# Optimization experiments

Measured on AMD Instinct MI355X. Metric: run time of the kernel, lower is better.

The kernel has to match this reference:

```python
import jax, jax.numpy as jnp
import numpy as np

DIM = 1024
STATE = 256
B, S = 4, 4096

def setup_inputs() -> dict:
    key = jax.random.key(0)
    ks = jax.random.split(key, 8)
    sc_b = 1.0 / np.sqrt(DIM)
    sc_c = 1.0 / np.sqrt(STATE)
    return {
        "x": jax.random.normal(ks[0], (B, S, DIM), dtype=jnp.float32),
        "A": jax.random.normal(ks[1], (STATE,), dtype=jnp.float32) * 0.02,
        "B_w": jax.random.uniform(ks[2], (STATE, DIM), minval=-sc_b, maxval=sc_b),
        "B_b": jax.random.uniform(ks[3], (STATE,), minval=-sc_b, maxval=sc_b),
        "C_w": jax.random.uniform(ks[4], (DIM, STATE), minval=-sc_c, maxval=sc_c),
        "C_b": jax.random.uniform(ks[5], (DIM,), minval=-sc_c, maxval=sc_c),
        "D_w": jax.random.uniform(ks[6], (DIM, DIM), minval=-sc_b, maxval=sc_b),
        "D_b": jax.random.uniform(ks[7], (DIM,), minval=-sc_b, maxval=sc_b),
    }

def reference(x, A, B_w, B_b, C_w, C_b, D_w, D_b):
    # Precompute input projections in batch (the per-step loop only needs state*A + Bu)
    Bu = jnp.einsum('bsd,nd->bsn', x, B_w) + B_b          # [B,S,STATE]
    Du = jnp.einsum('bsd,ed->bse', x, D_w) + D_b          # [B,S,DIM]
    Aexp = jnp.exp(A)[None, :]                             # [1,STATE]
    state0 = jnp.zeros((x.shape[0], A.shape[0]), dtype=x.dtype)

    def step(state, bu_t):
        state = jnp.tanh(state * Aexp + bu_t)
        return state, state

    _, states = jax.lax.scan(step, state0, jnp.swapaxes(Bu, 0, 1))  # [S,B,STATE]
    states = jnp.swapaxes(states, 0, 1)                              # [B,S,STATE]
    y = jnp.einsum('bsn,en->bse', states, C_w) + C_b + Du
    return y
```

## Files before the change

kernel.cpp:

```cpp
#include <hip/hip_runtime.h>
#include <hip/hip_bf16.h>

#define DIM 1024
#define STATE 256
#define BATCH 4
#define SEQ 4096
#define M_TOT (BATCH * SEQ)

typedef short short8 __attribute__((ext_vector_type(8)));
typedef float f32x4 __attribute__((ext_vector_type(4)));

__device__ __forceinline__ unsigned short f2bf(float f) {
  unsigned int u = __float_as_uint(f);
  u += 0x7fff + ((u >> 16) & 1);
  return (unsigned short)(u >> 16);
}

__device__ __forceinline__ void gl_lds16(const void* g, void* l) {
  __builtin_amdgcn_global_load_lds(
      (const __attribute__((address_space(1))) void*)g,
      (__attribute__((address_space(3))) void*)l, 16, 0, 0);
}

#define C2F 2.8853900817779268f
#define LOG2EF 1.4426950408889634f
#define VMC(N) asm volatile("s_waitcnt vmcnt(" #N ")" ::: "memory")

__global__ __launch_bounds__(256) void convert_w(
    const float* __restrict__ A, const float* __restrict__ Bw,
    const float* __restrict__ Bb, const float* __restrict__ Cw,
    const float* __restrict__ Cb, const float* __restrict__ Dw,
    const float* __restrict__ Db, unsigned short* __restrict__ bwb,
    unsigned short* __restrict__ wob, float* __restrict__ bb2,
    float* __restrict__ mP2, float* __restrict__ cbdb) {
  const int bx = blockIdx.x;
  const int t = threadIdx.x;
  if (bx < 256) {
    int c = t * 4;
    const float4 v = *(const float4*)(Bw + (size_t)bx * DIM + c);
    *(ushort4*)(bwb + (size_t)bx * DIM + c) =
        make_ushort4(f2bf(v.x), f2bf(v.y), f2bf(v.z), f2bf(v.w));
  } else if (bx < 256 + 1024) {
    int e = bx - 256;
    if (t < 64) {
      const float4 v = *(const float4*)(Cw + (size_t)e * STATE + t * 4);
      *(ushort4*)(wob + (size_t)e * 1280 + t * 4) =
          make_ushort4(f2bf(v.x), f2bf(v.y), f2bf(v.z), f2bf(v.w));
    }
    const float4 v = *(const float4*)(Dw + (size_t)e * DIM + t * 4);
    *(ushort4*)(wob + (size_t)e * 1280 + 256 + t * 4) =
        make_ushort4(f2bf(v.x), f2bf(v.y), f2bf(v.z), f2bf(v.w));
  } else {
    const float P = C2F * __builtin_amdgcn_exp2f(A[t] * LOG2EF);
    bb2[t] = fmaf(Bb[t], C2F, P);
    mP2[t] = -2.0f * P;
#pragma unroll
    for (int k = 0; k < 4; ++k) {
      const int i = t * 4 + k;
      cbdb[i] = Cb[i] + Db[i];
    }
  }
}

__global__ __launch_bounds__(256, 3) void gemm_GX(
    const float* __restrict__ x,
    const unsigned short* __restrict__ bwb,
    float* __restrict__ G,
    const float* __restrict__ bb2,
    unsigned short* __restrict__ xb)
{
  __shared__ char AsB[32768];
  __shared__ char BsB[16384];

  const int tid = threadIdx.x;
  const int wave = tid >> 6;
  const int lane = tid & 63;
  const int lr = lane & 15;
  const int lk = lane >> 4;
  const int wr = wave >> 1;
  const int wc = wave & 1;

  const int bs = (blockIdx.x & 7) * 32 + (blockIdx.x >> 3);
  const int mtile = bs >> 1;
  const int ntile = bs & 1;
  const int m0 = mtile * 128;
  const int n0 = ntile * 128;

  f32x4 acc[4][4];
#pragma unroll
  for (int i = 0; i < 4; ++i)
#pragma unroll
    for (int j = 0; j < 4; ++j) acc[i][j] = (f32x4){0.f, 0.f, 0.f, 0.f};

  const char* xB  = (const char*)x;
  const char* bwB = (const char*)bwb;
  char* xbB = (char*)xb;

  for (int k0 = 0; k0 < 1024; k0 += 64) {
#pragma unroll
    for (int i = 0; i < 8; ++i) {
      const int s = i * 256 + tid;
      const int r = s >> 4;
      const int c = (s & 15) ^ (r & 7);
      gl_lds16(xB + (size_t)(m0 + r) * 4096 + (size_t)k0 * 4 + c * 16,
               AsB + i * 4096 + wave * 1024);
    }
#pragma unroll
    for (int i = 0; i < 4; ++i) {
      const int s = i * 256 + tid;
      const int r = s >> 3;
      const int c = (s & 7) ^ (r & 7);
      gl_lds16(bwB + (size_t)(n0 + r) * 2048 + (size_t)k0 * 2 + c * 16,
               BsB + i * 4096 + wave * 1024);
    }
    __syncthreads();

#pragma unroll
    for (int kk = 0; kk < 2; ++kk) {
      short8 af[4], bfr[4];
#pragma unroll
      for (int f = 0; f < 4; ++f) {
        const int ra = wr * 64 + f * 16 + lr;
        const int swa = ra & 7;
        const f32x4 a0 = *(const f32x4*)(AsB + ra * 256 + (((kk * 8 + 2 * lk) ^ swa) << 4));
        const f32x4 a1 = *(const f32x4*)(AsB + ra * 256 + (((kk * 8 + 2 * lk + 1) ^ swa) << 4));
        short8 v;
#pragma unroll
        for (int j = 0; j < 4; ++j) {
          v[j]     = (short)f2bf(a0[j]);
          v[4 + j] = (short)f2bf(a1[j]);
        }
        af[f] = v;
        const int rb = wc * 64 + f * 16 + lr;
        bfr[f] = *(const short8*)(BsB + rb * 128 + (((kk * 4 + lk) ^ (rb & 7)) << 4));
      }
#pragma unroll
      for (int i = 0; i < 4; ++i)
#pragma unroll
        for (int j = 0; j < 4; ++j)
          acc[i][j] = __builtin_amdgcn_mfma_f32_16x16x32_bf16(af[i], bfr[j], acc[i][j], 0, 0, 0);
    }

    if (ntile == 0) {
#pragma unroll
      for (int i = 0; i < 4; ++i) {
        const int o = i * 256 + tid;
        const int r = o >> 3;
        const int oc = o & 7;
        const int sw = r & 7;
        const f32x4 a0 = *(const f32x4*)(AsB + r * 256 + (((2 * oc) ^ sw) << 4));
        const f32x4 a1 = *(const f32x4*)(AsB + r * 256 + (((2 * oc + 1) ^ sw) << 4));
        short8 v;
#pragma unroll
        for (int j = 0; j < 4; ++j) {
          v[j]     = (short)f2bf(a0[j]);
          v[4 + j] = (short)f2bf(a1[j]);
        }
        *(short8*)(xbB + (size_t)(m0 + r) * 2048 + (size_t)k0 * 2 + oc * 16) = v;
      }
    }
    __syncthreads();
  }

#pragma unroll
  for (int fi = 0; fi < 4; ++fi)
#pragma unroll
    for (int fj = 0; fj < 4; ++fj)
#pragma unroll
      for (int j = 0; j < 4; ++j) {
        const int rg = m0 + wr * 64 + fi * 16 + lk * 4 + j;
        const int cg = n0 + wc * 64 + fj * 16 + lr;
        G[(size_t)rg * STATE + cg] = fmaf(acc[fi][fj][j], C2F, bb2[cg]);
      }
}

__global__ __launch_bounds__(256) void scan_kernel(
    const float* __restrict__ G, const float* __restrict__ mP2arr,
    unsigned short* __restrict__ states) {
  const int b = blockIdx.x >> 6;
  const int chunk = blockIdx.x & 63;
  const int n = threadIdx.x;
  const int t0 = chunk * 64;
  const int start = (t0 > 128) ? (t0 - 128) : 0;
  const int nw = t0 - start;
  const int total = nw + 64;

  const float* g = G + ((size_t)b * SEQ + start) * STATE + n;
  unsigned short* q = states + ((size_t)b * SEQ + start) * STATE + n;
  const float mP2 = mP2arr[n];

  float r = 0.5f;
  constexpr int CH = 16;
  float cur[CH], nxt[CH];
#pragma unroll
  for (int j = 0; j < CH; ++j) cur[j] = g[(size_t)j * STATE];

  const int NC = total / CH;
  for (int c = 0; c < NC; ++c) {
    if (c + 1 < NC) {
      const float* pn = g + (size_t)(c + 1) * CH * STATE;
#pragma unroll
      for (int j = 0; j < CH; ++j) nxt[j] = pn[(size_t)j * STATE];
    }
    if (c * CH >= nw) {
      unsigned short* qc = q + (size_t)c * CH * STATE;
#pragma unroll
      for (int j = 0; j < CH; ++j) {
        const float t = fmaf(mP2, r, cur[j]);
        const float e = __builtin_amdgcn_exp2f(t);
        r = __builtin_amdgcn_rcpf(1.0f + e);
        const float s = fmaf(-2.0f, r, 1.0f);
        qc[(size_t)j * STATE] = f2bf(s);
      }
    } else {
#pragma unroll
      for (int j = 0; j < CH; ++j) {
        const float t = fmaf(mP2, r, cur[j]);
        const float e = __builtin_amdgcn_exp2f(t);
        r = __builtin_amdgcn_rcpf(1.0f + e);
      }
    }
    if (c + 1 < NC) {
#pragma unroll
      for (int j = 0; j < CH; ++j) cur[j] = nxt[j];
    }
  }
}

#define PH(TILE, Q, STG, VMST)                                                 \
  do {                                                                         \
    const char* As = lds + ((TILE) & 1) * 32768;                               \
    const char* Bs = lds + 65536 + ((TILE) & 1) * 32768;                       \
    if ((Q) == 0) {                                                            \
      _Pragma("unroll") for (int fj = 0; fj < 4; ++fj) {                       \
        const int r = wn * 64 + fj * 16 + lr;                                  \
        _Pragma("unroll") for (int kk = 0; kk < 2; ++kk)                       \
          bfr[fj][kk] = *(const short8*)(Bs + r * 128 +                        \
                                         (((kk * 4 + lk) ^ (r & 7)) << 4));    \
      }                                                                        \
    }                                                                          \
    short8 af[2][2];                                                           \
    _Pragma("unroll") for (int fl = 0; fl < 2; ++fl) {                         \
      const int r = wm * 128 + (Q) * 32 + fl * 16 + lr;                        \
      _Pragma("unroll") for (int kk = 0; kk < 2; ++kk)                         \
        af[fl][kk] = *(const short8*)(As + r * 128 +                           \
                                      (((kk * 4 + lk) ^ (r & 7)) << 4));       \
    }                                                                          \
    STG;                                                                       \
    if ((Q) == 0) asm volatile("s_waitcnt lgkmcnt(8)" ::: "memory");           \
    __builtin_amdgcn_s_barrier();                                              \
    __builtin_amdgcn_s_setprio(1);                                             \
    _Pragma("unroll") for (int kk = 0; kk < 2; ++kk)                           \
      _Pragma("unroll") for (int fl = 0; fl < 2; ++fl)                         \
        _Pragma("unroll") for (int fj = 0; fj < 4; ++fj)                       \
          acc[(Q) * 2 + fl][fj] = __builtin_amdgcn_mfma_f32_16x16x32_bf16(     \
              af[fl][kk], bfr[fj][kk], acc[(Q) * 2 + fl][fj], 0, 0, 0);        \
    __builtin_amdgcn_s_setprio(0);                                             \
    VMST;                                                                      \
    __builtin_amdgcn_s_barrier();                                              \
  } while (0)

__global__ __launch_bounds__(512, 2) void gemm_out(
    const unsigned short* __restrict__ stb,
    const unsigned short* __restrict__ xb,
    const unsigned short* __restrict__ wob,
    const float* __restrict__ cbdb,
    float* __restrict__ dout)
{
  __shared__ char lds[131072];

  const int tid = threadIdx.x;
  const int wave = tid >> 6;
  const int lane = tid & 63;
  const int lr = lane & 15;
  const int lk = lane >> 4;
  const int wm = wave >> 2;
  const int wn = wave & 3;

  const int bs = ((blockIdx.x & 7) << 5) | (blockIdx.x >> 3);
  const int m0 = (bs >> 2) * 256;
  const int n0 = (bs & 3) * 256;

  const char* stbB = (const char*)stb;
  const char* xbB  = (const char*)xb;
  const char* wobB = (const char*)wob;

  f32x4 acc[8][4];
#pragma unroll
  for (int i = 0; i < 8; ++i)
#pragma unroll
    for (int j = 0; j < 4; ++j) acc[i][j] = (f32x4){0.f, 0.f, 0.f, 0.f};

  auto stageA = [&](int kt, int h) {
    if (kt >= 20) return;
    const char* base;
    size_t str;
    size_t colb;
    if (kt < 4) { base = stbB; str = 512;  colb = (size_t)kt * 128; }
    else        { base = xbB;  str = 2048; colb = (size_t)(kt - 4) * 128; }
    base += (size_t)m0 * str;
#pragma unroll
    for (int i2 = 0; i2 < 2; ++i2) {
      const int s = i2 * 512 + tid;
      const int r = s >> 3;
      const int cl = (s & 7) ^ (r & 7);
      gl_lds16(base + (size_t)(h * 128 + r) * str + colb + cl * 16,
               lds + ((kt & 1) * 32768) + h * 16384 + i2 * 8192 + wave * 1024);
    }
  };
  auto stageB = [&](int kt, int h) {
    if (kt >= 20) return;
#pragma unroll
    for (int i2 = 0; i2 < 2; ++i2) {
      const int s = i2 * 512 + tid;
      const int r = s >> 3;
      const int cl = (s & 7) ^ (r & 7);
      gl_lds16(wobB + (size_t)(n0 + h * 128 + r) * 2560 + (size_t)kt * 128 + cl * 16,
               lds + 65536 + ((kt & 1) * 32768) + h * 16384 + i2 * 8192 + wave * 1024);
    }
  };

  stageA(0, 0); stageA(0, 1);
  stageB(0, 0); stageB(0, 1);
  stageB(1, 0); stageB(1, 1);
  VMC(4);
  __builtin_amdgcn_s_barrier();

  short8 bfr[4][2];
  for (int i = 0; i < 10; ++i) {
    const int e = 2 * i, o = e + 1;
    PH(e, 0, stageA(o, 0), );
    PH(e, 1, stageA(o, 1), );
    PH(e, 2, stageB(e + 2, 0), );
    PH(e, 3, stageB(e + 2, 1), if (i == 9) { VMC(0); } else { VMC(4); });
    PH(o, 0, stageA(e + 2, 0), );
    PH(o, 1, stageA(e + 2, 1), );
    PH(o, 2, stageB(o + 2, 0), );
    PH(o, 3, stageB(o + 2, 1), VMC(4));
  }

#pragma unroll
  for (int fj = 0; fj < 4; ++fj) {
    const int col = n0 + wn * 64 + fj * 16 + lr;
    const float cb = cbdb[col];
#pragma unroll
    for (int m = 0; m < 8; ++m) {
      const int rowb = m0 + wm * 128 + m * 16 + lk * 4;
#pragma unroll
      for (int j = 0; j < 4; ++j)
        dout[(size_t)(rowb + j) * DIM + col] = acc[m][fj][j] + cb;
    }
  }
}

extern "C" void kernel_launch(void* const* d_in, const int* in_sizes, int n_in,
                              void* d_out, int out_size, void* d_ws, size_t ws_size,
                              hipStream_t stream) {
  const float* x  = (const float*)d_in[0];
  const float* A  = (const float*)d_in[1];
  const float* Bw = (const float*)d_in[2];
  const float* Bb = (const float*)d_in[3];
  const float* Cw = (const float*)d_in[4];
  const float* Cb = (const float*)d_in[5];
  const float* Dw = (const float*)d_in[6];
  const float* Db = (const float*)d_in[7];
  float* dout = (float*)d_out;

  char* ws = (char*)d_ws;
  unsigned short* xb   = (unsigned short*)(ws);
  unsigned short* bwb  = (unsigned short*)(ws + 33554432);
  unsigned short* wob  = (unsigned short*)(ws + 34078720);
  float*          G    = (float*)         (ws + 36700160);
  unsigned short* stb  = (unsigned short*)(ws + 53477376);
  float*          bb2  = (float*)         (ws + 61865984);
  float*          mP2  = (float*)         (ws + 61867008);
  float*          cbdb = (float*)         (ws + 61868032);

  convert_w<<<256 + 1024 + 1, 256, 0, stream>>>(
      A, Bw, Bb, Cw, Cb, Dw, Db, bwb, wob, bb2, mP2, cbdb);
  gemm_GX<<<256, 256, 0, stream>>>(x, bwb, G, bb2, xb);
  scan_kernel<<<BATCH * 64, 256, 0, stream>>>(G, mP2, stb);
  gemm_out<<<256, 512, 0, stream>>>(stb, xb, wob, cbdb, dout);
}
```

Measured before the change: 100.6 us.

## Restructure x·B_w GEMM into 32-row full-N tiles with triple-buffered async loads

The first GEMM now gives each block 32 rows and all 256 state columns, so x is read and converted to bf16 once, with no duplication across N tiles. The grid doubles to 512 blocks. K is split into 32 steps of 32, staged through a 3-slot LDS ring with global_load_lds and vmcnt waits, replacing the load/sync/compute/sync loop. The bf16 copy of x is now written straight from the converted MFMA fragments by wave 0. The cost is more B_w re-reads per block, smaller per-iteration MFMA work, and a 60KB LDS footprint that limits occupancy to two blocks.

```diff
diff --git a/kernel.cpp b/kernel.cpp
--- a/kernel.cpp
+++ b/kernel.cpp
@@ -62,33 +62,25 @@
   }
 }
 
-__global__ __launch_bounds__(256, 3) void gemm_GX(
+__global__ __launch_bounds__(256, 2) void gemm_GX(
     const float* __restrict__ x,
     const unsigned short* __restrict__ bwb,
     float* __restrict__ G,
     const float* __restrict__ bb2,
     unsigned short* __restrict__ xb)
 {
-  __shared__ char AsB[32768];
-  __shared__ char BsB[16384];
+  __shared__ char lds[61440];
 
   const int tid = threadIdx.x;
   const int wave = tid >> 6;
   const int lane = tid & 63;
   const int lr = lane & 15;
   const int lk = lane >> 4;
-  const int wr = wave >> 1;
-  const int wc = wave & 1;
-
-  const int bs = (blockIdx.x & 7) * 32 + (blockIdx.x >> 3);
-  const int mtile = bs >> 1;
-  const int ntile = bs & 1;
-  const int m0 = mtile * 128;
-  const int n0 = ntile * 128;
-
-  f32x4 acc[4][4];
-#pragma unroll
-  for (int i = 0; i < 4; ++i)
+  const int m0 = blockIdx.x * 32;
+
+  f32x4 acc[2][4];
+#pragma unroll
+  for (int i = 0; i < 2; ++i)
 #pragma unroll
     for (int j = 0; j < 4; ++j) acc[i][j] = (f32x4){0.f, 0.f, 0.f, 0.f};
 
@@ -96,81 +88,83 @@
   const char* bwB = (const char*)bwb;
   char* xbB = (char*)xb;
 
-  for (int k0 = 0; k0 < 1024; k0 += 64) {
-#pragma unroll
-    for (int i = 0; i < 8; ++i) {
-      const int s = i * 256 + tid;
-      const int r = s >> 4;
-      const int c = (s & 15) ^ (r & 7);
-      gl_lds16(xB + (size_t)(m0 + r) * 4096 + (size_t)k0 * 4 + c * 16,
-               AsB + i * 4096 + wave * 1024);
+  auto stage = [&](int kt) {
+    if (kt >= 32) return;
+    char* slot = lds + (kt % 3) * 20480;
+    {
+      const int r = tid >> 3;
+      const int c = (tid & 7) ^ (r & 7);
+      gl_lds16(xB + (size_t)(m0 + r) * 4096 + (size_t)kt * 128 + c * 16,
+               slot + wave * 1024);
     }
 #pragma unroll
     for (int i = 0; i < 4; ++i) {
       const int s = i * 256 + tid;
-      const int r = s >> 3;
-      const int c = (s & 7) ^ (r & 7);
-      gl_lds16(bwB + (size_t)(n0 + r) * 2048 + (size_t)k0 * 2 + c * 16,
-               BsB + i * 4096 + wave * 1024);
-    }
-    __syncthreads();
-
-#pragma unroll
-    for (int kk = 0; kk < 2; ++kk) {
-      short8 af[4], bfr[4];
-#pragma unroll
-      for (int f = 0; f < 4; ++f) {
-        const int ra = wr * 64 + f * 16 + lr;
-        const int swa = ra & 7;
-        const f32x4 a0 = *(const f32x4*)(AsB + ra * 256 + (((kk * 8 + 2 * lk) ^ swa) << 4));
-        const f32x4 a1 = *(const f32x4*)(AsB + ra * 256 + (((kk * 8 + 2 * lk + 1) ^ swa) << 4));
-        short8 v;
-#pragma unroll
-        for (int j = 0; j < 4; ++j) {
-          v[j]     = (short)f2bf(a0[j]);
-          v[4 + j] = (short)f2bf(a1[j]);
-        }
-        af[f] = v;
-        const int rb = wc * 64 + f * 16 + lr;
-        bfr[f] = *(const short8*)(BsB + rb * 128 + (((kk * 4 + lk) ^ (rb & 7)) << 4));
-      }
-#pragma unroll
-      for (int i = 0; i < 4; ++i)
-#pragma unroll
-        for (int j = 0; j < 4; ++j)
-          acc[i][j] = __builtin_amdgcn_mfma_f32_16x16x32_bf16(af[i], bfr[j], acc[i][j], 0, 0, 0);
-    }
-
-    if (ntile == 0) {
-#pragma unroll
-      for (int i = 0; i < 4; ++i) {
-        const int o = i * 256 + tid;
-        const int r = o >> 3;
-        const int oc = o & 7;
-        const int sw = r & 7;
-        const f32x4 a0 = *(const f32x4*)(AsB + r * 256 + (((2 * oc) ^ sw) << 4));
-        const f32x4 a1 = *(const f32x4*)(AsB + r * 256 + (((2 * oc + 1) ^ sw) << 4));
-        short8 v;
-#pragma unroll
-        for (int j = 0; j < 4; ++j) {
-          v[j]     = (short)f2bf(a0[j]);
-          v[4 + j] = (short)f2bf(a1[j]);
-        }
-        *(short8*)(xbB + (size_t)(m0 + r) * 2048 + (size_t)k0 * 2 + oc * 16) = v;
-      }
-    }
-    __syncthreads();
-  }
-
-#pragma unroll
-  for (int fi = 0; fi < 4; ++fi)
+      const int r = s >> 2;
+      const int c = s & 3;
+      gl_lds16(bwB + (size_t)r * 2048 + (size_t)kt * 64 + c * 16,
+               slot + 4096 + i * 4096 + wave * 1024);
+    }
+  };
+
+  stage(0); stage(1);
+  VMC(5);
+  __builtin_amdgcn_s_barrier();
+
+  for (int t = 0; t < 32; ++t) {
+    stage(t + 2);
+
+    const char* As = lds + (t % 3) * 20480;
+    const char* Bs = As + 4096;
+
+    short8 af[2], bfr[4];
+#pragma unroll
+    for (int f = 0; f < 2; ++f) {
+      const int row = f * 16 + lr;
+      const int sw = row & 7;
+      const f32x4 a0 = *(const f32x4*)(As + row * 128 + (((2 * lk)     ^ sw) << 4));
+      const f32x4 a1 = *(const f32x4*)(As + row * 128 + (((2 * lk + 1) ^ sw) << 4));
+      short8 v;
+#pragma unroll
+      for (int j = 0; j < 4; ++j) {
+        v[j]     = (short)f2bf(a0[j]);
+        v[4 + j] = (short)f2bf(a1[j]);
+      }
+      af[f] = v;
+    }
+#pragma unroll
+    for (int fj = 0; fj < 4; ++fj) {
+      const int rb = wave * 64 + fj * 16 + lr;
+      bfr[fj] = *(const short8*)(Bs + rb * 64 + (lk << 4));
+    }
+#pragma unroll
+    for (int f = 0; f < 2; ++f)
+#pragma unroll
+      for (int fj = 0; fj < 4; ++fj)
+        acc[f][fj] = __builtin_amdgcn_mfma_f32_16x16x32_bf16(af[f], bfr[fj], acc[f][fj], 0, 0, 0);
+
+    if (wave == 0) {
+#pragma unroll
+      for (int f = 0; f < 2; ++f) {
+        const int row = f * 16 + lr;
+        *(short8*)(xbB + (size_t)(m0 + row) * 2048 + (size_t)t * 64 + lk * 16) = af[f];
+      }
+      if (t < 30) { VMC(7); } else { VMC(0); }
+    } else {
+      if (t < 30) { VMC(5); } else { VMC(0); }
+    }
+    __builtin_amdgcn_s_barrier();
+  }
+
+#pragma unroll
+  for (int f = 0; f < 2; ++f)
 #pragma unroll
     for (int fj = 0; fj < 4; ++fj)
 #pragma unroll
       for (int j = 0; j < 4; ++j) {
-        const int rg = m0 + wr * 64 + fi * 16 + lk * 4 + j;
-        const int cg = n0 + wc * 64 + fj * 16 + lr;
-        G[(size_t)rg * STATE + cg] = fmaf(acc[fi][fj][j], C2F, bb2[cg]);
+        const int rg = m0 + f * 16 + lk * 4 + j;
+        const int cg = wave * 64 + fj * 16 + lr;
+        G[(size_t)rg * STATE + cg] = fmaf(acc[f][fj][j], C2F, bb2[cg]);
       }
 }
 
@@ -378,7 +372,7 @@
 
   convert_w<<<256 + 1024 + 1, 256, 0, stream>>>(
       A, Bw, Bb, Cw, Cb, Dw, Db, bwb, wob, bb2, mP2, cbdb);
-  gemm_GX<<<256, 256, 0, stream>>>(x, bwb, G, bb2, xb);
+  gemm_GX<<<512, 256, 0, stream>>>(x, bwb, G, bb2, xb);
   scan_kernel<<<BATCH * 64, 256, 0, stream>>>(G, mP2, stb);
   gemm_out<<<256, 512, 0, stream>>>(stb, xb, wob, cbdb, dout);
 }
```

Result: faster. 96.10 us (-4.5%).
